# Kernel tuning notes

Measured on AMD Instinct MI355X. Metric: run time of the kernel, lower is better.

## Reference

```python
import jax, jax.numpy as jnp
import numpy as np

N = 50000
E = 640000
D = 128
H = 512
LN_EPS = 1e-5


def setup_inputs() -> dict:
    key = jax.random.key(0)
    ks = jax.random.split(key, 6)
    x = jax.random.normal(ks[0], (N, D), dtype=jnp.float32)
    edge_index = jax.random.randint(ks[1], (2, E), 0, N, dtype=jnp.int64)
    edge_dist = jax.random.uniform(ks[2], (E,), dtype=jnp.float32)
    # true out-degrees of src so degree normalization is realistic
    degrees = jax.ops.segment_sum(jnp.ones((E,), jnp.float32), edge_index[0], num_segments=N)
    W1 = jax.random.normal(ks[3], (2 * D + 2, H), dtype=jnp.float32) * (1.0 / np.sqrt(2 * D + 2))
    b1 = jnp.zeros((H,), jnp.float32)
    W2 = jax.random.normal(ks[4], (H, D), dtype=jnp.float32) * (1.0 / np.sqrt(H))
    b2 = jnp.zeros((D,), jnp.float32)
    gamma = jnp.ones((D,), jnp.float32)
    beta = jnp.zeros((D,), jnp.float32)
    return {"x": x, "W1": W1, "b1": b1, "W2": W2, "b2": b2,
            "gamma": gamma, "beta": beta,
            "edge_index": edge_index, "edge_dist": edge_dist, "degrees": degrees}


def reference(x, W1, b1, W2, b2, gamma, beta, edge_index, edge_dist, degrees):
    n = x.shape[0]
    src, dst = edge_index[0], edge_index[1]
    # gather neighbor features, scatter-add into source nodes
    msg = x[dst]                                             # [E, D]
    agg = jax.ops.segment_sum(msg, src, num_segments=n)      # [N, D]
    deg = jnp.maximum(degrees, 1.0)                          # clamp_min(1.0)
    agg = agg / deg[:, None]
    dist_sum = jax.ops.segment_sum(edge_dist, src, num_segments=n)  # [N]
    mean_dist = dist_sum / deg                               # [N]
    feat = jnp.concatenate([x, agg, degrees[:, None], mean_dist[:, None]], axis=-1)  # [N, 2D+2]
    h = jax.nn.relu(feat @ W1 + b1)
    out = h @ W2 + b2
    y = x + out
    mu = jnp.mean(y, axis=-1, keepdims=True)
    var = jnp.var(y, axis=-1, keepdims=True)
    return (y - mu) / jnp.sqrt(var + LN_EPS) * gamma + beta
```

## Files before the change

### kernel.cpp

```cpp
#include <hip/hip_runtime.h>
#include <hip/hip_bf16.h>

#define NN 50000
#define EE 640000
#define LN_EPS 1e-5f
#define KD 272
#define KB 544
#define NBK2 782
#define CH 4096

typedef __bf16 bf16x8 __attribute__((ext_vector_type(8)));
typedef float f32x16 __attribute__((ext_vector_type(16)));

static __device__ __forceinline__ unsigned short f2bf(float f) {
    return __builtin_bit_cast(unsigned short, (__bf16)f);
}
static __device__ __forceinline__ float bflo(unsigned int u) {
    return __builtin_bit_cast(float, u << 16);
}
static __device__ __forceinline__ float bfhi(unsigned int u) {
    return __builtin_bit_cast(float, u & 0xffff0000u);
}

__global__ __launch_bounds__(256) void cast_x(const float* __restrict__ x,
                                              unsigned short* __restrict__ xbf) {
    int i = blockIdx.x * 256 + threadIdx.x;
    const float4* s = (const float4*)x + (size_t)i * 2;
    float4 a = s[0], b = s[1];
    unsigned short o[8] = { f2bf(a.x), f2bf(a.y), f2bf(a.z), f2bf(a.w),
                            f2bf(b.x), f2bf(b.y), f2bf(b.z), f2bf(b.w) };
    *(uint4*)(xbf + (size_t)i * 8) = *(const uint4*)o;
}

__global__ __launch_bounds__(256) void prep_weights(const float* __restrict__ W1,
                                                    const float* __restrict__ b1,
                                                    const float* __restrict__ W2,
                                                    unsigned short* __restrict__ Wimg) {
    int idx = blockIdx.x * 256 + threadIdx.x;
    int ct = idx / 12800;
    int r = idx - ct * 12800;
    float v = 0.f;
    if (r < 8704) {
        int slot = r >> 8;
        int c = (r >> 3) & 31;
        int e = r & 7;
        int k = slot * 8 + e;
        int col = ct * 32 + c;
        if (k < 258) v = W1[(size_t)k * 512 + col];
        else if (k == 258) v = b1[col];
    } else {
        int r2 = r - 8704;
        int slot = r2 >> 10;
        int c2 = (r2 >> 3) & 127;
        int e = r2 & 7;
        int k = ct * 32 + slot * 8 + e;
        v = W2[(size_t)k * 128 + c2];
    }
    Wimg[idx] = f2bf(v);
}

__global__ __launch_bounds__(256) void scanA(const float* __restrict__ degrees,
                                             int* __restrict__ blocksum) {
    __shared__ int wsum[4];
    int i = blockIdx.x * 256 + threadIdx.x;
    int v = (i < NN) ? (int)(degrees[i] + 0.5f) : 0;
    int s = v;
    for (int d = 1; d < 64; d <<= 1) s += __shfl_xor(s, d, 64);
    if ((threadIdx.x & 63) == 0) wsum[threadIdx.x >> 6] = s;
    __syncthreads();
    if (threadIdx.x == 0) blocksum[blockIdx.x] = wsum[0] + wsum[1] + wsum[2] + wsum[3];
}

__global__ __launch_bounds__(256) void scanB(const int* __restrict__ blocksum,
                                             int* __restrict__ blockoff, int nb) {
    __shared__ int wsum[4];
    int tid = threadIdx.x;
    int v = (tid < nb) ? blocksum[tid] : 0;
    int lane = tid & 63, wid = tid >> 6;
    int inc = v;
    for (int d = 1; d < 64; d <<= 1) { int t = __shfl_up(inc, d, 64); if (lane >= d) inc += t; }
    if (lane == 63) wsum[wid] = inc;
    __syncthreads();
    int add = 0;
    for (int w = 0; w < wid; w++) add += wsum[w];
    inc += add;
    if (tid < nb) blockoff[tid] = inc - v;
}

__global__ __launch_bounds__(256) void scanC(const float* __restrict__ degrees,
                                             const int* __restrict__ blockoff,
                                             int* __restrict__ start,
                                             int* __restrict__ gcur) {
    __shared__ int wsum[4];
    int tid = threadIdx.x;
    int i = blockIdx.x * 256 + tid;
    int v = (i < NN) ? (int)(degrees[i] + 0.5f) : 0;
    int lane = tid & 63, wid = tid >> 6;
    int inc = v;
    for (int d = 1; d < 64; d <<= 1) { int t = __shfl_up(inc, d, 64); if (lane >= d) inc += t; }
    if (lane == 63) wsum[wid] = inc;
    __syncthreads();
    int add = blockoff[blockIdx.x];
    for (int w = 0; w < wid; w++) add += wsum[w];
    int excl = add + inc - v;
    if (i < NN) {
        start[i] = excl;
        if ((i & 63) == 0) gcur[i >> 6] = excl;
    }
}

__global__ __launch_bounds__(256) void bin_kernel(const int* __restrict__ ei,
                                                  const float* __restrict__ edist,
                                                  int* __restrict__ gcur,
                                                  unsigned* __restrict__ recs1,
                                                  float* __restrict__ dist) {
    __shared__ int cnt[NBK2], off[NBK2], gb[NBK2], c2[NBK2];
    __shared__ int wsum[4];
    __shared__ unsigned stage[CH];
    __shared__ int gtg[CH];
    int tid = threadIdx.x, lane = tid & 63, wid = tid >> 6;
    int e0 = blockIdx.x * CH;
    int nval = EE - e0; if (nval > CH) nval = CH;

    for (int i = tid; i < NBK2; i += 256) { cnt[i] = 0; c2[i] = 0; }
    __syncthreads();
#pragma unroll
    for (int k = 0; k < CH / 256; k++) {
        int e = e0 + k * 256 + tid;
        if (e < EE) atomicAdd(&cnt[ei[e] >> 6], 1);
    }
    __syncthreads();
    {
        int v[4], s = 0;
#pragma unroll
        for (int j = 0; j < 4; j++) {
            int idx = tid * 4 + j;
            v[j] = (idx < NBK2) ? cnt[idx] : 0;
            s += v[j];
        }
        int inc = s;
        for (int d = 1; d < 64; d <<= 1) { int t = __shfl_up(inc, d, 64); if (lane >= d) inc += t; }
        if (lane == 63) wsum[wid] = inc;
        __syncthreads();
        int base = 0;
        for (int w = 0; w < wid; w++) base += wsum[w];
        int ex = base + inc - s;
#pragma unroll
        for (int j = 0; j < 4; j++) {
            int idx = tid * 4 + j;
            if (idx < NBK2) off[idx] = ex;
            ex += v[j];
        }
    }
    __syncthreads();
    for (int i = tid; i < NBK2; i += 256) {
        int c = cnt[i];
        gb[i] = c ? atomicAdd(&gcur[i], c) : 0;
    }
    __syncthreads();
#pragma unroll
    for (int k = 0; k < CH / 256; k++) {
        int e = e0 + k * 256 + tid;
        if (e < EE) {
            int s = ei[e];
            int d = ei[EE + e];
            atomicAdd(dist + s, edist[e]);
            int b = s >> 6;
            int p = atomicAdd(&c2[b], 1);
            int slot = off[b] + p;
            stage[slot] = (unsigned)d | ((unsigned)(s & 63) << 16);
            gtg[slot] = gb[b] + p;
        }
    }
    __syncthreads();
    for (int i = tid; i < nval; i += 256)
        recs1[gtg[i]] = stage[i];
}

__global__ __launch_bounds__(256) void subsort_kernel(const unsigned* __restrict__ recs1,
                                                      const int* __restrict__ start,
                                                      unsigned short* __restrict__ recs2) {
    __shared__ int cur[64];
    int bkt = blockIdx.x, tid = threadIdx.x;
    int bstart = start[bkt * 64];
    int bend = (bkt == NBK2 - 1) ? EE : start[(bkt + 1) * 64];
    if (tid < 64) {
        int node = bkt * 64 + tid;
        cur[tid] = (node < NN) ? start[node] : EE;
    }
    __syncthreads();
    for (int i = bstart + tid; i < bend; i += 256) {
        unsigned r = recs1[i];
        int p = atomicAdd(&cur[(r >> 16) & 63], 1);
        recs2[p] = (unsigned short)(r & 0xffffu);
    }
}

__global__ __launch_bounds__(256) void aggfeat_kernel(const unsigned short* __restrict__ xbf,
                                                      const int* __restrict__ start,
                                                      const float* __restrict__ degrees,
                                                      const unsigned short* __restrict__ recs2,
                                                      const float* __restrict__ dist,
                                                      unsigned short* __restrict__ featbf) {
    int tid = threadIdx.x;
    int node = blockIdx.x * 4 + (tid >> 6);
    int lane = tid & 63;
    if (node >= NN) return;
    int st = start[node];
    int cnt = (int)(degrees[node] + 0.5f);
    float a0 = 0.f, a1 = 0.f;
    for (int base = 0; base < cnt; base += 64) {
        int rem = cnt - base;
        int nv = rem < 64 ? rem : 64;
        int didx = (lane < nv) ? (int)recs2[st + base + lane] : 0;
        int j = 0;
        for (; j + 4 <= nv; j += 4) {
            int d0 = __shfl(didx, j,     64);
            int d1 = __shfl(didx, j + 1, 64);
            int d2 = __shfl(didx, j + 2, 64);
            int d3 = __shfl(didx, j + 3, 64);
            unsigned x0 = *(const unsigned*)(xbf + (size_t)d0 * 128 + lane * 2);
            unsigned x1 = *(const unsigned*)(xbf + (size_t)d1 * 128 + lane * 2);
            unsigned x2 = *(const unsigned*)(xbf + (size_t)d2 * 128 + lane * 2);
            unsigned x3 = *(const unsigned*)(xbf + (size_t)d3 * 128 + lane * 2);
            a0 += bflo(x0) + bflo(x1) + bflo(x2) + bflo(x3);
            a1 += bfhi(x0) + bfhi(x1) + bfhi(x2) + bfhi(x3);
        }
        for (; j < nv; j++) {
            int dj = __shfl(didx, j, 64);
            unsigned xv = *(const unsigned*)(xbf + (size_t)dj * 128 + lane * 2);
            a0 += bflo(xv);
            a1 += bfhi(xv);
        }
    }
    float dg = degrees[node];
    float degc = fmaxf(dg, 1.0f);
    float inv = 1.0f / degc;
    unsigned short* row = featbf + (size_t)node * KD;
    *(unsigned int*)(row + lane * 2) = *(const unsigned int*)(xbf + (size_t)node * 128 + lane * 2);
    unsigned short o2[2] = { f2bf(a0 * inv), f2bf(a1 * inv) };
    *(unsigned int*)(row + 128 + lane * 2) = *(const unsigned int*)o2;
    if (lane < 4) {
        unsigned short t4[4] = { 0, 0, 0, 0 };
        if (lane == 0) { t4[0] = f2bf(dg); t4[1] = f2bf(dist[node] * inv); t4[2] = f2bf(1.0f); }
        *(uint2*)(row + 256 + lane * 4) = *(const uint2*)t4;
    }
}

__global__ __launch_bounds__(128, 2) void fused_mlp_ln(const unsigned short* __restrict__ featbf,
                                                       const unsigned short* __restrict__ Wimg,
                                                       const float* __restrict__ x,
                                                       const float* __restrict__ b2,
                                                       const float* __restrict__ gamma,
                                                       const float* __restrict__ beta,
                                                       float* __restrict__ out) {
    __shared__ __align__(16) unsigned char lds[25600];

    int tid = threadIdx.x;
    int lane = tid & 63;
    int ln = lane & 31, hi = lane >> 5;
    int wave = tid >> 6;
    int rowbase = blockIdx.x * 64 + wave * 32;
    int gr = rowbase + ln;

    bf16x8 ffr[17];
    if (gr < NN) {
        const unsigned char* fp = (const unsigned char*)featbf + (size_t)gr * KB + hi * 16;
#pragma unroll
        for (int ks = 0; ks < 17; ks++)
            ffr[ks] = *(const bf16x8*)(fp + ks * 32);
    } else {
#pragma unroll
        for (int ks = 0; ks < 17; ks++) ffr[ks] = (bf16x8)(__bf16)0.0f;
    }

    f32x16 acc2[4] = {};

    const uint4* img = (const uint4*)Wimg;
    uint4* lb = (uint4*)lds;

    for (int ct = 0; ct < 16; ct++) {
        const uint4* src = img + ct * 1600;
        for (int idx = tid; idx < 1600; idx += 128)
            lb[idx] = src[idx];
        __syncthreads();

        f32x16 acc1 = {};
#pragma unroll
        for (int ks = 0; ks < 17; ks++) {
            bf16x8 af = *(const bf16x8*)(lds + (2 * ks + hi) * 512 + ln * 16);
            acc1 = __builtin_amdgcn_mfma_f32_32x32x16_bf16(af, ffr[ks], acc1, 0, 0, 0);
        }

        unsigned int dw[4][2];
#pragma unroll
        for (int g = 0; g < 4; g++)
#pragma unroll
            for (int i = 0; i < 2; i++) {
                float lo = fmaxf(acc1[g * 4 + 2 * i], 0.f);
                float hf = fmaxf(acc1[g * 4 + 2 * i + 1], 0.f);
                dw[g][i] = (unsigned int)f2bf(lo) | ((unsigned int)f2bf(hf) << 16);
            }

        const unsigned char* B2c = lds + 17408;
#pragma unroll
        for (int w = 0; w < 2; w++) {
            unsigned int sL0 = dw[2 * w][0],     sL1 = dw[2 * w][1];
            unsigned int sH0 = dw[2 * w + 1][0], sH1 = dw[2 * w + 1][1];
            unsigned int send0 = hi ? sL0 : sH0;
            unsigned int send1 = hi ? sL1 : sH1;
            unsigned int r0 = (unsigned int)__shfl_xor((int)send0, 32, 64);
            unsigned int r1 = (unsigned int)__shfl_xor((int)send1, 32, 64);
            uint4 fd;
            fd.x = hi ? r0 : sL0;
            fd.y = hi ? r1 : sL1;
            fd.z = hi ? sH0 : r0;
            fd.w = hi ? sH1 : r1;
            bf16x8 hfr = __builtin_bit_cast(bf16x8, fd);
#pragma unroll
            for (int at = 0; at < 4; at++) {
                bf16x8 a2 = *(const bf16x8*)(B2c + (2 * w + hi) * 2048 + (at * 32 + ln) * 16);
                acc2[at] = __builtin_amdgcn_mfma_f32_32x32x16_bf16(a2, hfr, acc2[at], 0, 0, 0);
            }
        }
        __syncthreads();
    }

    bool rok = (gr < NN);
    float sum = 0.f, sq = 0.f;
#pragma unroll
    for (int at = 0; at < 4; at++)
#pragma unroll
        for (int g = 0; g < 4; g++) {
            int c0 = at * 32 + g * 8 + hi * 4;
            float4 bq = *(const float4*)(b2 + c0);
            float4 xq = rok ? *(const float4*)(x + (size_t)gr * 128 + c0) : make_float4(0, 0, 0, 0);
            float vb[4] = { bq.x, bq.y, bq.z, bq.w };
            float vx[4] = { xq.x, xq.y, xq.z, xq.w };
#pragma unroll
            for (int m = 0; m < 4; m++) {
                float v = acc2[at][g * 4 + m] + vb[m] + vx[m];
                acc2[at][g * 4 + m] = v;
                sum += v;
                sq += v * v;
            }
        }
    sum += __shfl_xor(sum, 32, 64);
    sq  += __shfl_xor(sq, 32, 64);
    float mu = sum * (1.0f / 128.0f);
    float var = sq * (1.0f / 128.0f) - mu * mu;
    float rs = rsqrtf(var + LN_EPS);
    if (rok) {
        float* orow = out + (size_t)gr * 128;
#pragma unroll
        for (int at = 0; at < 4; at++)
#pragma unroll
            for (int g = 0; g < 4; g++) {
                int c0 = at * 32 + g * 8 + hi * 4;
                float4 gq = *(const float4*)(gamma + c0);
                float4 be = *(const float4*)(beta + c0);
                float4 o;
                o.x = (acc2[at][g * 4 + 0] - mu) * rs * gq.x + be.x;
                o.y = (acc2[at][g * 4 + 1] - mu) * rs * gq.y + be.y;
                o.z = (acc2[at][g * 4 + 2] - mu) * rs * gq.z + be.z;
                o.w = (acc2[at][g * 4 + 3] - mu) * rs * gq.w + be.w;
                *(float4*)(orow + c0) = o;
            }
    }
}

extern "C" void kernel_launch(void* const* d_in, const int* in_sizes, int n_in,
                              void* d_out, int out_size, void* d_ws, size_t ws_size,
                              hipStream_t stream) {
    const float* x       = (const float*)d_in[0];
    const float* W1      = (const float*)d_in[1];
    const float* b1      = (const float*)d_in[2];
    const float* W2      = (const float*)d_in[3];
    const float* b2      = (const float*)d_in[4];
    const float* gamma   = (const float*)d_in[5];
    const float* beta    = (const float*)d_in[6];
    const int*   ei      = (const int*)d_in[7];
    const float* edist   = (const float*)d_in[8];
    const float* degrees = (const float*)d_in[9];
    float* out = (float*)d_out;

    char* ws = (char*)d_ws;
    size_t off = 0;
    auto alloc = [&](size_t bytes) {
        void* p = ws + off;
        off = (off + bytes + 255) & ~(size_t)255;
        return p;
    };
    unsigned* recs1         = (unsigned*)alloc((size_t)EE * 4);
    unsigned short* recs2   = (unsigned short*)alloc((size_t)EE * 2);
    int* start              = (int*)alloc((size_t)NN * 4);
    int* gcur               = (int*)alloc(NBK2 * 4);
    int* blocksum           = (int*)alloc(256 * 4);
    int* blockoff           = (int*)alloc(256 * 4);
    float* dist             = (float*)alloc((size_t)NN * 4);
    unsigned short* xbf     = (unsigned short*)alloc((size_t)NN * 128 * 2);
    unsigned short* featbf  = (unsigned short*)alloc((size_t)NN * KD * 2);
    unsigned short* Wimg    = (unsigned short*)alloc((size_t)204800 * 2);

    const int NB = (NN + 255) / 256;

    hipMemsetAsync(dist, 0, (size_t)NN * 4, stream);
    cast_x<<<3125, 256, 0, stream>>>(x, xbf);
    prep_weights<<<800, 256, 0, stream>>>(W1, b1, W2, Wimg);
    scanA<<<NB, 256, 0, stream>>>(degrees, blocksum);
    scanB<<<1, 256, 0, stream>>>(blocksum, blockoff, NB);
    scanC<<<NB, 256, 0, stream>>>(degrees, blockoff, start, gcur);
    bin_kernel<<<(EE + CH - 1) / CH, 256, 0, stream>>>(ei, edist, gcur, recs1, dist);
    subsort_kernel<<<NBK2, 256, 0, stream>>>(recs1, start, recs2);
    aggfeat_kernel<<<(NN + 3) / 4, 256, 0, stream>>>(xbf, start, degrees, recs2, dist, featbf);
    fused_mlp_ln<<<(NN + 63) / 64, 128, 0, stream>>>(featbf, Wimg, x, b2, gamma, beta, out);
}
```

Baseline: 268.3 us.

## Widen MLP hidden-column tiles to 64 and use 4-wave blocks sharing LDS weights

Measured after the change: 238.9 us. -10.9%, faster.

```diff
diff --git a/kernel.cpp b/kernel.cpp
--- a/kernel.cpp
+++ b/kernel.cpp
@@ -37,23 +37,23 @@
                                                     const float* __restrict__ W2,
                                                     unsigned short* __restrict__ Wimg) {
     int idx = blockIdx.x * 256 + threadIdx.x;
-    int ct = idx / 12800;
-    int r = idx - ct * 12800;
+    int ct = idx / 25600;
+    int r = idx - ct * 25600;
     float v = 0.f;
-    if (r < 8704) {
-        int slot = r >> 8;
-        int c = (r >> 3) & 31;
+    if (r < 17408) {
+        int slot = r >> 9;
+        int c = (r >> 3) & 63;
         int e = r & 7;
         int k = slot * 8 + e;
-        int col = ct * 32 + c;
+        int col = ct * 64 + c;
         if (k < 258) v = W1[(size_t)k * 512 + col];
         else if (k == 258) v = b1[col];
     } else {
-        int r2 = r - 8704;
+        int r2 = r - 17408;
         int slot = r2 >> 10;
         int c2 = (r2 >> 3) & 127;
         int e = r2 & 7;
-        int k = ct * 32 + slot * 8 + e;
+        int k = ct * 64 + slot * 8 + e;
         v = W2[(size_t)k * 128 + c2];
     }
     Wimg[idx] = f2bf(v);
@@ -247,20 +247,19 @@
     }
 }
 
-__global__ __launch_bounds__(128, 2) void fused_mlp_ln(const unsigned short* __restrict__ featbf,
+__global__ __launch_bounds__(256, 2) void fused_mlp_ln(const unsigned short* __restrict__ featbf,
                                                        const unsigned short* __restrict__ Wimg,
                                                        const float* __restrict__ x,
                                                        const float* __restrict__ b2,
                                                        const float* __restrict__ gamma,
                                                        const float* __restrict__ beta,
                                                        float* __restrict__ out) {
-    __shared__ __align__(16) unsigned char lds[25600];
+    __shared__ __align__(16) unsigned char lds[51200];
 
     int tid = threadIdx.x;
-    int lane = tid & 63;
+    int wave = tid >> 6, lane = tid & 63;
     int ln = lane & 31, hi = lane >> 5;
-    int wave = tid >> 6;
-    int rowbase = blockIdx.x * 64 + wave * 32;
+    int rowbase = blockIdx.x * 128 + wave * 32;
     int gr = rowbase + ln;
 
     bf16x8 ffr[17];
@@ -279,50 +278,58 @@
     const uint4* img = (const uint4*)Wimg;
     uint4* lb = (uint4*)lds;
 
-    for (int ct = 0; ct < 16; ct++) {
-        const uint4* src = img + ct * 1600;
-        for (int idx = tid; idx < 1600; idx += 128)
+    for (int ct = 0; ct < 8; ct++) {
+        const uint4* src = img + ct * 3200;
+        for (int idx = tid; idx < 3200; idx += 256)
             lb[idx] = src[idx];
         __syncthreads();
 
-        f32x16 acc1 = {};
+        f32x16 acc1[2] = {};
 #pragma unroll
         for (int ks = 0; ks < 17; ks++) {
-            bf16x8 af = *(const bf16x8*)(lds + (2 * ks + hi) * 512 + ln * 16);
-            acc1 = __builtin_amdgcn_mfma_f32_32x32x16_bf16(af, ffr[ks], acc1, 0, 0, 0);
-        }
-
-        unsigned int dw[4][2];
-#pragma unroll
-        for (int g = 0; g < 4; g++)
-#pragma unroll
-            for (int i = 0; i < 2; i++) {
-                float lo = fmaxf(acc1[g * 4 + 2 * i], 0.f);
-                float hf = fmaxf(acc1[g * 4 + 2 * i + 1], 0.f);
-                dw[g][i] = (unsigned int)f2bf(lo) | ((unsigned int)f2bf(hf) << 16);
+#pragma unroll
+            for (int t = 0; t < 2; t++) {
+                bf16x8 af = *(const bf16x8*)(lds + (2 * ks + hi) * 1024 + (t * 32 + ln) * 16);
+                acc1[t] = __builtin_amdgcn_mfma_f32_32x32x16_bf16(af, ffr[ks], acc1[t], 0, 0, 0);
             }
-
-        const unsigned char* B2c = lds + 17408;
-#pragma unroll
-        for (int w = 0; w < 2; w++) {
-            unsigned int sL0 = dw[2 * w][0],     sL1 = dw[2 * w][1];
-            unsigned int sH0 = dw[2 * w + 1][0], sH1 = dw[2 * w + 1][1];
-            unsigned int send0 = hi ? sL0 : sH0;
-            unsigned int send1 = hi ? sL1 : sH1;
-            unsigned int r0 = (unsigned int)__shfl_xor((int)send0, 32, 64);
-            unsigned int r1 = (unsigned int)__shfl_xor((int)send1, 32, 64);
-            uint4 fd;
-            fd.x = hi ? r0 : sL0;
-            fd.y = hi ? r1 : sL1;
-            fd.z = hi ? sH0 : r0;
-            fd.w = hi ? sH1 : r1;
-            bf16x8 hfr = __builtin_bit_cast(bf16x8, fd);
-#pragma unroll
-            for (int at = 0; at < 4; at++) {
-                bf16x8 a2 = *(const bf16x8*)(B2c + (2 * w + hi) * 2048 + (at * 32 + ln) * 16);
-                acc2[at] = __builtin_amdgcn_mfma_f32_32x32x16_bf16(a2, hfr, acc2[at], 0, 0, 0);
+        }
+
+        unsigned int dw[2][4][2];
+#pragma unroll
+        for (int t = 0; t < 2; t++)
+#pragma unroll
+            for (int g = 0; g < 4; g++)
+#pragma unroll
+                for (int i = 0; i < 2; i++) {
+                    float lo = fmaxf(acc1[t][g * 4 + 2 * i], 0.f);
+                    float hf = fmaxf(acc1[t][g * 4 + 2 * i + 1], 0.f);
+                    dw[t][g][i] = (unsigned int)f2bf(lo) | ((unsigned int)f2bf(hf) << 16);
+                }
+
+        const unsigned char* B2c = lds + 34816;
+#pragma unroll
+        for (int t = 0; t < 2; t++)
+#pragma unroll
+            for (int w = 0; w < 2; w++) {
+                int ks2 = t * 2 + w;
+                unsigned int sL0 = dw[t][2 * w][0],     sL1 = dw[t][2 * w][1];
+                unsigned int sH0 = dw[t][2 * w + 1][0], sH1 = dw[t][2 * w + 1][1];
+                unsigned int send0 = hi ? sL0 : sH0;
+                unsigned int send1 = hi ? sL1 : sH1;
+                unsigned int r0 = (unsigned int)__shfl_xor((int)send0, 32, 64);
+                unsigned int r1 = (unsigned int)__shfl_xor((int)send1, 32, 64);
+                uint4 fd;
+                fd.x = hi ? r0 : sL0;
+                fd.y = hi ? r1 : sL1;
+                fd.z = hi ? sH0 : r0;
+                fd.w = hi ? sH1 : r1;
+                bf16x8 hfr = __builtin_bit_cast(bf16x8, fd);
+#pragma unroll
+                for (int at = 0; at < 4; at++) {
+                    bf16x8 a2 = *(const bf16x8*)(B2c + (2 * ks2 + hi) * 2048 + (at * 32 + ln) * 16);
+                    acc2[at] = __builtin_amdgcn_mfma_f32_32x32x16_bf16(a2, hfr, acc2[at], 0, 0, 0);
+                }
             }
-        }
         __syncthreads();
     }
 
@@ -413,5 +420,5 @@
     bin_kernel<<<(EE + CH - 1) / CH, 256, 0, stream>>>(ei, edist, gcur, recs1, dist);
     subsort_kernel<<<NBK2, 256, 0, stream>>>(recs1, start, recs2);
     aggfeat_kernel<<<(NN + 3) / 4, 256, 0, stream>>>(xbf, start, degrees, recs2, dist, featbf);
-    fused_mlp_ln<<<(NN + 63) / 64, 128, 0, stream>>>(featbf, Wimg, x, b2, gamma, beta, out);
-}
+    fused_mlp_ln<<<(NN + 127) / 128, 256, 0, stream>>>(featbf, Wimg, x, b2, gamma, beta, out);
+}
```
